# Kernel tuning notes

Measured on AMD Instinct MI355X. Metric: run time of the kernel, lower is better.

Reference implementation:

```python
import jax, jax.numpy as jnp
import numpy as np

S, T, D, H, DQ, F = 2048, 2048, 1024, 16, 1024, 4096
HD = DQ // H


def _layernorm(x, w, b, eps=1e-5):
    mu = jnp.mean(x, axis=-1, keepdims=True)
    var = jnp.mean((x - mu) ** 2, axis=-1, keepdims=True)
    return (x - mu) / jnp.sqrt(var + eps) * w + b


def _attention(q_in, kv_in, mask, wq, bq, wk, bk, wv, bv, wo, bo):
    # q_in: [Sq, D], kv_in: [Sk, D]
    q = (q_in @ wq + bq).reshape(-1, H, HD).transpose(1, 0, 2)   # [H, Sq, hd]
    k = (kv_in @ wk + bk).reshape(-1, H, HD).transpose(1, 0, 2)  # [H, Sk, hd]
    v = (kv_in @ wv + bv).reshape(-1, H, HD).transpose(1, 0, 2)
    scale = jnp.sqrt(jnp.asarray(HD, dtype=q.dtype))
    scores = jnp.einsum('hqd,hkd->hqk', q, k) / scale            # [H, Sq, Sk]
    if mask is not None:
        scores = jnp.where(mask, scores, jnp.finfo(scores.dtype).min)
    attn = jax.nn.softmax(scores, axis=-1)
    ctx = jnp.einsum('hqk,hkd->hqd', attn, v)                    # [H, Sq, hd]
    ctx = ctx.transpose(1, 0, 2).reshape(-1, H * HD)             # [Sq, DQ]
    return ctx @ wo + bo


def setup_inputs() -> dict:
    key = jax.random.key(0)
    ks = jax.random.split(key, 20)

    def lin(kk, fan_in, shape):
        return jax.random.normal(kk, shape, dtype=jnp.float32) / np.sqrt(fan_in)

    inp = {
        'inputs': jax.random.normal(ks[0], (S, D), dtype=jnp.float32),
        'encoder_outputs': jax.random.normal(ks[1], (T, D), dtype=jnp.float32),
        'self_attention_mask': jnp.tril(jnp.ones((S, S), dtype=bool)),
        'cross_attention_mask': jnp.ones((S, T), dtype=bool),
        'ln1_w': jnp.ones((D,), jnp.float32), 'ln1_b': jnp.zeros((D,), jnp.float32),
        'ln2_w': jnp.ones((D,), jnp.float32), 'ln2_b': jnp.zeros((D,), jnp.float32),
        'ln3_w': jnp.ones((D,), jnp.float32), 'ln3_b': jnp.zeros((D,), jnp.float32),
        'sa_wq': lin(ks[2], D, (D, DQ)), 'sa_bq': jnp.zeros((DQ,), jnp.float32),
        'sa_wk': lin(ks[3], D, (D, DQ)), 'sa_bk': jnp.zeros((DQ,), jnp.float32),
        'sa_wv': lin(ks[4], D, (D, DQ)), 'sa_bv': jnp.zeros((DQ,), jnp.float32),
        'sa_wo': lin(ks[5], DQ, (DQ, D)), 'sa_bo': jnp.zeros((D,), jnp.float32),
        'ca_wq': lin(ks[6], D, (D, DQ)), 'ca_bq': jnp.zeros((DQ,), jnp.float32),
        'ca_wk': lin(ks[7], D, (D, DQ)), 'ca_bk': jnp.zeros((DQ,), jnp.float32),
        'ca_wv': lin(ks[8], D, (D, DQ)), 'ca_bv': jnp.zeros((DQ,), jnp.float32),
        'ca_wo': lin(ks[9], DQ, (DQ, D)), 'ca_bo': jnp.zeros((D,), jnp.float32),
        'mlp_wi': lin(ks[10], D, (D, F)), 'mlp_bi': jnp.zeros((F,), jnp.float32),
        'mlp_wo': lin(ks[11], F, (F, D)), 'mlp_bo': jnp.zeros((D,), jnp.float32),
    }
    return inp


def reference(inputs, encoder_outputs, self_attention_mask, cross_attention_mask,
              ln1_w, ln1_b, ln2_w, ln2_b, ln3_w, ln3_b,
              sa_wq, sa_bq, sa_wk, sa_bk, sa_wv, sa_bv, sa_wo, sa_bo,
              ca_wq, ca_bq, ca_wk, ca_bk, ca_wv, ca_bv, ca_wo, ca_bo,
              mlp_wi, mlp_bi, mlp_wo, mlp_bo):
    # pre-norm self-attention
    n1 = _layernorm(inputs, ln1_w, ln1_b)
    x = inputs + _attention(n1, n1, self_attention_mask,
                            sa_wq, sa_bq, sa_wk, sa_bk, sa_wv, sa_bv, sa_wo, sa_bo)
    # pre-norm cross-attention (kv from encoder, not normalized)
    n2 = _layernorm(x, ln2_w, ln2_b)
    x = x + _attention(n2, encoder_outputs, cross_attention_mask,
                       ca_wq, ca_bq, ca_wk, ca_bk, ca_wv, ca_bv, ca_wo, ca_bo)
    # pre-norm MLP
    n3 = _layernorm(x, ln3_w, ln3_b)
    h = jax.nn.relu(n3 @ mlp_wi + mlp_bi)
    return x + (h @ mlp_wo + mlp_bo)
```

## Files before the change

### kernel.cpp

```cpp
#include <hip/hip_runtime.h>


#define S_LEN 2048
#define T_LEN 2048
#define D_DIM 1024
#define H_NUM 16
#define DQ_DIM 1024
#define F_DIM 4096
#define HD_DIM 64

typedef _Float16 f16x8 __attribute__((ext_vector_type(8)));
typedef _Float16 f16x4 __attribute__((ext_vector_type(4)));
typedef float f32x4 __attribute__((ext_vector_type(4)));

__device__ __forceinline__ void split1(float x, _Float16& h, _Float16& l) {
    _Float16 hh = (_Float16)x;
    h = hh;
    l = (_Float16)((x - (float)hh) * 2048.0f);
}

__device__ __forceinline__ void gload16(const void* g, void* l) {
    __builtin_amdgcn_global_load_lds(
        (const __attribute__((address_space(1))) void*)g,
        (__attribute__((address_space(3))) void*)l, 16, 0, 0);
}

struct WC8 { const float* w[8]; _Float16* th[8]; _Float16* tl[8]; };

__global__ __launch_bounds__(256)
void wconv_kernel(WC8 a, int K, int N) {
    __shared__ __align__(16) _Float16 th[64][72], tl[64][72];
    const float* W = a.w[blockIdx.z];
    _Float16* Th = a.th[blockIdx.z];
    _Float16* Tl = a.tl[blockIdx.z];
    int n0 = blockIdx.x * 64, k0 = blockIdx.y * 64;
    int t = threadIdx.x;
#pragma unroll
    for (int i = 0; i < 4; ++i) {
        int idx = i * 256 + t;
        int kk = idx >> 4, nq = idx & 15;
        float4 w4 = *(const float4*)(W + (size_t)(k0 + kk) * N + n0 + nq * 4);
        _Float16 h, l;
        split1(w4.x, h, l); th[nq * 4 + 0][kk] = h; tl[nq * 4 + 0][kk] = l;
        split1(w4.y, h, l); th[nq * 4 + 1][kk] = h; tl[nq * 4 + 1][kk] = l;
        split1(w4.z, h, l); th[nq * 4 + 2][kk] = h; tl[nq * 4 + 2][kk] = l;
        split1(w4.w, h, l); th[nq * 4 + 3][kk] = h; tl[nq * 4 + 3][kk] = l;
    }
    __syncthreads();
#pragma unroll
    for (int i = 0; i < 2; ++i) {
        int idx = i * 256 + t;
        int nn = idx >> 3, kq = idx & 7;
        *(f16x8*)(Th + (size_t)(n0 + nn) * K + k0 + kq * 8) = *(const f16x8*)&th[nn][kq * 8];
        *(f16x8*)(Tl + (size_t)(n0 + nn) * K + k0 + kq * 8) = *(const f16x8*)&tl[nn][kq * 8];
    }
}

__global__ __launch_bounds__(256)
void esplit_kernel(const float* __restrict__ x, _Float16* __restrict__ hi,
                   _Float16* __restrict__ lo) {
    size_t i = ((size_t)blockIdx.x * 256 + threadIdx.x) * 4;
    float4 v = *(const float4*)(x + i);
    f16x4 hv, lv; _Float16 h, l;
    split1(v.x, h, l); hv[0] = h; lv[0] = l;
    split1(v.y, h, l); hv[1] = h; lv[1] = l;
    split1(v.z, h, l); hv[2] = h; lv[2] = l;
    split1(v.w, h, l); hv[3] = h; lv[3] = l;
    *(f16x4*)(hi + i) = hv;
    *(f16x4*)(lo + i) = lv;
}

__global__ __launch_bounds__(256)
void ln_kernel(const float* __restrict__ x, const float* __restrict__ w,
               const float* __restrict__ b, _Float16* __restrict__ outh,
               _Float16* __restrict__ outl) {
    int row = blockIdx.x;
    int t = threadIdx.x;
    float4 v = ((const float4*)(x + (size_t)row * D_DIM))[t];
    float s = v.x + v.y + v.z + v.w;
    float ss = v.x * v.x + v.y * v.y + v.z * v.z + v.w * v.w;
#pragma unroll
    for (int m = 1; m < 64; m <<= 1) {
        s += __shfl_xor(s, m, 64);
        ss += __shfl_xor(ss, m, 64);
    }
    __shared__ float ps[4], pss[4];
    int wid = t >> 6;
    if ((t & 63) == 0) { ps[wid] = s; pss[wid] = ss; }
    __syncthreads();
    s = ps[0] + ps[1] + ps[2] + ps[3];
    ss = pss[0] + pss[1] + pss[2] + pss[3];
    float mu = s * (1.0f / D_DIM);
    float var = ss * (1.0f / D_DIM) - mu * mu;
    float rstd = rsqrtf(var + 1e-5f);
    float4 wv = ((const float4*)w)[t];
    float4 bv = ((const float4*)b)[t];
    f16x4 hv, lv; _Float16 h, l;
    split1((v.x - mu) * rstd * wv.x + bv.x, h, l); hv[0] = h; lv[0] = l;
    split1((v.y - mu) * rstd * wv.y + bv.y, h, l); hv[1] = h; lv[1] = l;
    split1((v.z - mu) * rstd * wv.z + bv.z, h, l); hv[2] = h; lv[2] = l;
    split1((v.w - mu) * rstd * wv.w + bv.w, h, l); hv[3] = h; lv[3] = l;
    *(f16x4*)(outh + (size_t)row * D_DIM + t * 4) = hv;
    *(f16x4*)(outl + (size_t)row * D_DIM + t * 4) = lv;
}

struct GemmArgs {
    const _Float16 *Ah[3], *Al[3];
    const _Float16 *Bh[3], *Bl[3];
    const float *bias[3];
    void *C0[3];
    void *C1[3];
    int trans[3];
};

template <int EPI, int BM>
__global__ __launch_bounds__(256, 2)
void gemm_kernel(GemmArgs ga, int M, int N, int K) {
    static_assert(BM == 64 || BM == 128, "BM");
    constexpr int MI = BM / 32;
    constexpr int ASZ = BM * 32;
    constexpr int BUFSZ = 2 * ASZ + 4096;
    int z = blockIdx.z;
    const _Float16* Ah = ga.Ah[z];
    const _Float16* Al = ga.Al[z];
    const _Float16* Bh = ga.Bh[z];
    const _Float16* Bl = ga.Bl[z];
    const float* bias = ga.bias[z];
    void* C0 = ga.C0[z];
    void* C1 = ga.C1[z];
    int tr = ga.trans[z];

    __shared__ __align__(16) _Float16 lds[2 * BUFSZ];

    int t = threadIdx.x;
    int m0 = blockIdx.y * BM, n0 = blockIdx.x * 64;
    int lane = t & 63, wid = t >> 6;
    int g = lane >> 4, l15 = lane & 15;
    int wm = wid >> 1, wn = wid & 1;

    f32x4 acc1[MI][2] = {};
    f32x4 acc2[MI][2] = {};

    const int nt = K / 32;

    auto stage = [&](int kt, int bi) {
        int k0 = kt * 32;
        _Float16* buf = &lds[bi * BUFSZ];
#pragma unroll
        for (int c = 0; c < BM / 64; ++c) {
            int chunk = c * 256 + t;
            int row = chunk >> 2, cc = chunk & 3;
            int so = k0 + ((cc ^ (row & 3)) << 3);
            gload16(Ah + (size_t)(m0 + row) * K + so, buf + chunk * 8);
            gload16(Al + (size_t)(m0 + row) * K + so, buf + ASZ + chunk * 8);
        }
        {
            int chunk = t;
            int row = chunk >> 2, cc = chunk & 3;
            int so = k0 + ((cc ^ (row & 3)) << 3);
            gload16(Bh + (size_t)(n0 + row) * K + so, buf + 2 * ASZ + chunk * 8);
            gload16(Bl + (size_t)(n0 + row) * K + so, buf + 2 * ASZ + 2048 + chunk * 8);
        }
    };

    stage(0, 0);
    for (int kt = 0; kt < nt; ++kt) {
        __syncthreads();
        if (kt + 1 < nt) stage(kt + 1, (kt + 1) & 1);
        const _Float16* buf = &lds[(kt & 1) * BUFSZ];
        f16x8 ah[MI], al[MI], bh[2], bl[2];
#pragma unroll
        for (int mi = 0; mi < MI; ++mi) {
            int row = wm * (BM / 2) + mi * 16 + l15;
            int cof = row * 32 + ((g ^ (row & 3)) << 3);
            ah[mi] = *(const f16x8*)&buf[cof];
            al[mi] = *(const f16x8*)&buf[ASZ + cof];
        }
#pragma unroll
        for (int ni = 0; ni < 2; ++ni) {
            int row = wn * 32 + ni * 16 + l15;
            int cof = row * 32 + ((g ^ (row & 3)) << 3);
            bh[ni] = *(const f16x8*)&buf[2 * ASZ + cof];
            bl[ni] = *(const f16x8*)&buf[2 * ASZ + 2048 + cof];
        }
#pragma unroll
        for (int mi = 0; mi < MI; ++mi)
#pragma unroll
            for (int ni = 0; ni < 2; ++ni) {
                acc1[mi][ni] = __builtin_amdgcn_mfma_f32_16x16x32_f16(ah[mi], bh[ni], acc1[mi][ni], 0, 0, 0);
                acc2[mi][ni] = __builtin_amdgcn_mfma_f32_16x16x32_f16(ah[mi], bl[ni], acc2[mi][ni], 0, 0, 0);
                acc2[mi][ni] = __builtin_amdgcn_mfma_f32_16x16x32_f16(al[mi], bh[ni], acc2[mi][ni], 0, 0, 0);
            }
    }

#pragma unroll
    for (int ni = 0; ni < 2; ++ni) {
        int col = n0 + wn * 32 + ni * 16 + l15;
        float bb = bias[col];
#pragma unroll
        for (int mi = 0; mi < MI; ++mi) {
            int row0 = m0 + wm * (BM / 2) + mi * 16 + g * 4;
            float vr[4];
#pragma unroll
            for (int r = 0; r < 4; ++r)
                vr[r] = acc1[mi][ni][r] + acc2[mi][ni][r] * (1.0f / 2048.0f) + bb;
            if constexpr (EPI == 0) {
                if (tr) {
                    f16x4 tv;
#pragma unroll
                    for (int r = 0; r < 4; ++r) tv[r] = (_Float16)vr[r];
                    *(f16x4*)((_Float16*)C0 + (size_t)col * M + row0) = tv;
                } else {
#pragma unroll
                    for (int r = 0; r < 4; ++r)
                        ((_Float16*)C0)[(size_t)(row0 + r) * N + col] = (_Float16)vr[r];
                }
            } else if constexpr (EPI == 1) {
#pragma unroll
                for (int r = 0; r < 4; ++r) {
                    size_t off = (size_t)(row0 + r) * N + col;
                    ((float*)C0)[off] = vr[r] + ((const float*)C1)[off];
                }
            } else {
#pragma unroll
                for (int r = 0; r < 4; ++r) {
                    size_t off = (size_t)(row0 + r) * N + col;
                    _Float16 h, l;
                    split1(fmaxf(vr[r], 0.0f), h, l);
                    ((_Float16*)C0)[off] = h;
                    ((_Float16*)C1)[off] = l;
                }
            }
        }
    }
}

template <bool CAUSAL>
__global__ __launch_bounds__(512)
void flash_kernel(const _Float16* __restrict__ Qm, const _Float16* __restrict__ Km,
                  const _Float16* __restrict__ VT, _Float16* __restrict__ Oh,
                  _Float16* __restrict__ Ol, int Sk) {
    __shared__ __align__(16) _Float16 sK[64][64];
    __shared__ __align__(16) _Float16 sVT[64][64];
    __shared__ __align__(16) _Float16 sP[8][16][64];

    int t = threadIdx.x, lane = t & 63, wid = t >> 6;
    int g = lane >> 4, l15 = lane & 15;
    int h = blockIdx.y;
    int NT = Sk / 64;
    int ta = blockIdx.x, tb = NT - 1 - ta;
    int tidx = (wid < 4) ? ta : tb;
    int q0w = tidx * 64 + (wid & 3) * 16;
    int jendw = CAUSAL ? tidx : NT - 1;
    int jend = CAUSAL ? tb : NT - 1;

    f16x8 aq[2];
    {
        const _Float16* qp = Qm + (size_t)(q0w + l15) * DQ_DIM + h * HD_DIM;
#pragma unroll
        for (int ks = 0; ks < 2; ++ks) {
            f16x8 a = *(const f16x8*)(qp + ks * 32 + g * 8);
#pragma unroll
            for (int e = 0; e < 8; ++e) a[e] = a[e] * (_Float16)0.125f;
            aq[ks] = a;
        }
    }

    float m_[4] = {-1e30f, -1e30f, -1e30f, -1e30f};
    float l_[4] = {0.f, 0.f, 0.f, 0.f};
    f32x4 o[4] = {};

    int srow = t >> 3, scc = t & 7;
    f16x8 rk, rv;
    auto loadKV = [&](int jt) {
        int j0 = jt * 64;
        rk = *(const f16x8*)(Km + (size_t)(j0 + srow) * DQ_DIM + h * HD_DIM + scc * 8);
        rv = *(const f16x8*)(VT + (size_t)(h * HD_DIM + srow) * Sk + j0 + scc * 8);
    };

    loadKV(0);
    for (int jt = 0; jt <= jend; ++jt) {
        __syncthreads();
        {
            int sc_ = (scc ^ (srow & 7)) * 8;
            *(f16x8*)&sK[srow][sc_] = rk;
            *(f16x8*)&sVT[srow][sc_] = rv;
        }
        if (jt < jend) loadKV(jt + 1);
        __syncthreads();
        if (jt > jendw) continue;

        int j0 = jt * 64;
        f32x4 sc[4] = {};
#pragma unroll
        for (int cf = 0; cf < 4; ++cf)
#pragma unroll
            for (int ks = 0; ks < 2; ++ks) {
                f16x8 bk = *(const f16x8*)&sK[cf * 16 + l15][((ks * 4 + g) ^ (l15 & 7)) * 8];
                sc[cf] = __builtin_amdgcn_mfma_f32_16x16x32_f16(aq[ks], bk, sc[cf], 0, 0, 0);
            }
        if (CAUSAL && jt == tidx) {
#pragma unroll
            for (int cf = 0; cf < 4; ++cf)
#pragma unroll
                for (int r = 0; r < 4; ++r)
                    if (j0 + cf * 16 + l15 > q0w + g * 4 + r) sc[cf][r] = -1e30f;
        }
#pragma unroll
        for (int r = 0; r < 4; ++r) {
            float tmax = fmaxf(fmaxf(sc[0][r], sc[1][r]), fmaxf(sc[2][r], sc[3][r]));
#pragma unroll
            for (int mm = 1; mm < 16; mm <<= 1) tmax = fmaxf(tmax, __shfl_xor(tmax, mm, 64));
            float mn = fmaxf(m_[r], tmax);
            float corr = __expf(m_[r] - mn);
            float rs = 0.0f;
#pragma unroll
            for (int cf = 0; cf < 4; ++cf) {
                float p = __expf(sc[cf][r] - mn);
                sc[cf][r] = p;
                rs += p;
            }
#pragma unroll
            for (int mm = 1; mm < 16; mm <<= 1) rs += __shfl_xor(rs, mm, 64);
            l_[r] = l_[r] * corr + rs;
            m_[r] = mn;
#pragma unroll
            for (int hf = 0; hf < 4; ++hf) o[hf][r] *= corr;
        }
#pragma unroll
        for (int cf = 0; cf < 4; ++cf)
#pragma unroll
            for (int r = 0; r < 4; ++r) {
                int e = cf * 16 + l15;
                int se = (((e >> 3) ^ ((g * 4 + r) & 7)) << 3) | (e & 7);
                sP[wid][g * 4 + r][se] = (_Float16)sc[cf][r];
            }
#pragma unroll
        for (int ks = 0; ks < 2; ++ks) {
            f16x8 ap = *(const f16x8*)&sP[wid][l15][((ks * 4 + g) ^ (l15 & 7)) * 8];
#pragma unroll
            for (int hf = 0; hf < 4; ++hf) {
                f16x8 bv = *(const f16x8*)&sVT[hf * 16 + l15][((ks * 4 + g) ^ (l15 & 7)) * 8];
                o[hf] = __builtin_amdgcn_mfma_f32_16x16x32_f16(ap, bv, o[hf], 0, 0, 0);
            }
        }
    }

#pragma unroll
    for (int hf = 0; hf < 4; ++hf)
#pragma unroll
        for (int r = 0; r < 4; ++r) {
            int row = q0w + g * 4 + r;
            int col = h * HD_DIM + hf * 16 + l15;
            _Float16 hh, ll;
            split1(o[hf][r] / l_[r], hh, ll);
            Oh[(size_t)row * DQ_DIM + col] = hh;
            Ol[(size_t)row * DQ_DIM + col] = ll;
        }
}

#define MB(x) ((size_t)(x) * 1024 * 1024)

extern "C" void kernel_launch(void* const* d_in, const int* in_sizes, int n_in,
                              void* d_out, int out_size, void* d_ws, size_t ws_size,
                              hipStream_t stream) {
    const float* x_in = (const float*)d_in[0];
    const float* enc  = (const float*)d_in[1];
    const float* ln1w = (const float*)d_in[4];  const float* ln1b = (const float*)d_in[5];
    const float* ln2w = (const float*)d_in[6];  const float* ln2b = (const float*)d_in[7];
    const float* ln3w = (const float*)d_in[8];  const float* ln3b = (const float*)d_in[9];
    const float* sa_wq = (const float*)d_in[10]; const float* sa_bq = (const float*)d_in[11];
    const float* sa_wk = (const float*)d_in[12]; const float* sa_bk = (const float*)d_in[13];
    const float* sa_wv = (const float*)d_in[14]; const float* sa_bv = (const float*)d_in[15];
    const float* sa_wo = (const float*)d_in[16]; const float* sa_bo = (const float*)d_in[17];
    const float* ca_wq = (const float*)d_in[18]; const float* ca_bq = (const float*)d_in[19];
    const float* ca_wk = (const float*)d_in[20]; const float* ca_bk = (const float*)d_in[21];
    const float* ca_wv = (const float*)d_in[22]; const float* ca_bv = (const float*)d_in[23];
    const float* ca_wo = (const float*)d_in[24]; const float* ca_bo = (const float*)d_in[25];
    const float* mlp_wi = (const float*)d_in[26]; const float* mlp_bi = (const float*)d_in[27];
    const float* mlp_wo = (const float*)d_in[28]; const float* mlp_bo = (const float*)d_in[29];
    float* out = (float*)d_out;

    char* base = (char*)d_ws;
    float* X        = (float*)(base + MB(0));
    _Float16* Nbh   = (_Float16*)(base + MB(8));
    _Float16* Nbl   = (_Float16*)(base + MB(12));
    _Float16* Qb    = (_Float16*)(base + MB(16));
    _Float16* Kb    = (_Float16*)(base + MB(20));
    _Float16* VTb   = (_Float16*)(base + MB(24));
    _Float16* CXh   = (_Float16*)(base + MB(28));
    _Float16* CXl   = (_Float16*)(base + MB(32));
    _Float16* wT[8][2];
    const float* wsrc[8] = {sa_wq, sa_wk, sa_wv, sa_wo, ca_wq, ca_wk, ca_wv, ca_wo};
    for (int i = 0; i < 8; ++i) {
        wT[i][0] = (_Float16*)(base + MB(36 + 4 * i));
        wT[i][1] = (_Float16*)(base + MB(36 + 4 * i) + MB(2));
    }
    _Float16* wiTh  = (_Float16*)(base + MB(68));
    _Float16* wiTl  = (_Float16*)(base + MB(76));
    _Float16* woTh  = (_Float16*)(base + MB(84));
    _Float16* woTl  = (_Float16*)(base + MB(92));
    _Float16* ench  = (_Float16*)(base + MB(100));
    _Float16* encl  = (_Float16*)(base + MB(104));
    _Float16* Hbh   = (_Float16*)(base + MB(36));
    _Float16* Hbl   = (_Float16*)(base + MB(52));

    dim3 blk(256);
    dim3 fblk(512);

    {
        WC8 a;
        for (int i = 0; i < 8; ++i) { a.w[i] = wsrc[i]; a.th[i] = wT[i][0]; a.tl[i] = wT[i][1]; }
        wconv_kernel<<<dim3(16, 16, 8), blk, 0, stream>>>(a, D_DIM, DQ_DIM);
    }
    {
        WC8 a = {};
        a.w[0] = mlp_wi; a.th[0] = wiTh; a.tl[0] = wiTl;
        wconv_kernel<<<dim3(F_DIM / 64, D_DIM / 64, 1), blk, 0, stream>>>(a, D_DIM, F_DIM);
    }
    {
        WC8 a = {};
        a.w[0] = mlp_wo; a.th[0] = woTh; a.tl[0] = woTl;
        wconv_kernel<<<dim3(D_DIM / 64, F_DIM / 64, 1), blk, 0, stream>>>(a, F_DIM, D_DIM);
    }
    esplit_kernel<<<(size_t)T_LEN * D_DIM / 1024, blk, 0, stream>>>(enc, ench, encl);

    ln_kernel<<<S_LEN, blk, 0, stream>>>(x_in, ln1w, ln1b, Nbh, Nbl);
    {
        GemmArgs a = {};
        for (int z = 0; z < 3; ++z) { a.Ah[z] = Nbh; a.Al[z] = Nbl; }
        a.Bh[0] = wT[0][0]; a.Bl[0] = wT[0][1]; a.bias[0] = sa_bq; a.C0[0] = Qb;
        a.Bh[1] = wT[1][0]; a.Bl[1] = wT[1][1]; a.bias[1] = sa_bk; a.C0[1] = Kb;
        a.Bh[2] = wT[2][0]; a.Bl[2] = wT[2][1]; a.bias[2] = sa_bv; a.C0[2] = VTb;
        a.trans[2] = 1;
        gemm_kernel<0, 128><<<dim3(DQ_DIM / 64, S_LEN / 128, 3), blk, 0, stream>>>(
            a, S_LEN, DQ_DIM, D_DIM);
    }
    flash_kernel<true><<<dim3(S_LEN / 128, H_NUM), fblk, 0, stream>>>(Qb, Kb, VTb, CXh, CXl, S_LEN);
    {
        GemmArgs a = {};
        a.Ah[0] = CXh; a.Al[0] = CXl;
        a.Bh[0] = wT[3][0]; a.Bl[0] = wT[3][1]; a.bias[0] = sa_bo;
        a.C0[0] = X; a.C1[0] = (void*)x_in;
        gemm_kernel<1, 64><<<dim3(D_DIM / 64, S_LEN / 64, 1), blk, 0, stream>>>(
            a, S_LEN, D_DIM, DQ_DIM);
    }

    ln_kernel<<<S_LEN, blk, 0, stream>>>(X, ln2w, ln2b, Nbh, Nbl);
    {
        GemmArgs a = {};
        a.Ah[0] = Nbh;  a.Al[0] = Nbl;
        a.Ah[1] = ench; a.Al[1] = encl;
        a.Ah[2] = ench; a.Al[2] = encl;
        a.Bh[0] = wT[4][0]; a.Bl[0] = wT[4][1]; a.bias[0] = ca_bq; a.C0[0] = Qb;
        a.Bh[1] = wT[5][0]; a.Bl[1] = wT[5][1]; a.bias[1] = ca_bk; a.C0[1] = Kb;
        a.Bh[2] = wT[6][0]; a.Bl[2] = wT[6][1]; a.bias[2] = ca_bv; a.C0[2] = VTb;
        a.trans[2] = 1;
        gemm_kernel<0, 128><<<dim3(DQ_DIM / 64, S_LEN / 128, 3), blk, 0, stream>>>(
            a, S_LEN, DQ_DIM, D_DIM);
    }
    flash_kernel<false><<<dim3(S_LEN / 128, H_NUM), fblk, 0, stream>>>(Qb, Kb, VTb, CXh, CXl, T_LEN);
    {
        GemmArgs a = {};
        a.Ah[0] = CXh; a.Al[0] = CXl;
        a.Bh[0] = wT[7][0]; a.Bl[0] = wT[7][1]; a.bias[0] = ca_bo;
        a.C0[0] = X; a.C1[0] = X;
        gemm_kernel<1, 64><<<dim3(D_DIM / 64, S_LEN / 64, 1), blk, 0, stream>>>(
            a, S_LEN, D_DIM, DQ_DIM);
    }

    ln_kernel<<<S_LEN, blk, 0, stream>>>(X, ln3w, ln3b, Nbh, Nbl);
    {
        GemmArgs a = {};
        a.Ah[0] = Nbh; a.Al[0] = Nbl;
        a.Bh[0] = wiTh; a.Bl[0] = wiTl; a.bias[0] = mlp_bi;
        a.C0[0] = Hbh; a.C1[0] = Hbl;
        gemm_kernel<2, 128><<<dim3(F_DIM / 64, S_LEN / 128, 1), blk, 0, stream>>>(
            a, S_LEN, F_DIM, D_DIM);
    }
    {
        GemmArgs a = {};
        a.Ah[0] = Hbh; a.Al[0] = Hbl;
        a.Bh[0] = woTh; a.Bl[0] = woTl; a.bias[0] = mlp_bo;
        a.C0[0] = out; a.C1[0] = X;
        gemm_kernel<1, 64><<<dim3(D_DIM / 64, S_LEN / 64, 1), blk, 0, stream>>>(
            a, S_LEN, D_DIM, F_DIM);
    }

    (void)in_sizes; (void)n_in; (void)out_size; (void)ws_size;
}
```

Baseline: 576.4 us.

## Use 128x128 GEMM tiles and split-K for output projections with reduce kernel

Enlarges every GEMM tile to 128x128, with a 4x4 MFMA sub-tile per wave, to raise operand reuse from LDS. The LDS swizzle changes to match. The N=1024 output projections (attention out and MLP down) become a two-way split-K writing fp32 partials. A new elementwise kernel then adds the partials, the bias and the residual. This keeps enough blocks for occupancy with the larger tiles, at the cost of extra partial-sum memory traffic, one more launch and higher register pressure.

Measured after the change: 585.0 us. No clear change (+1.5%).

```diff
diff --git a/kernel.cpp b/kernel.cpp
--- a/kernel.cpp
+++ b/kernel.cpp
@@ -113,53 +113,48 @@
     int trans[3];
 };
 
-template <int EPI, int BM>
+template <int EPI>
 __global__ __launch_bounds__(256, 2)
 void gemm_kernel(GemmArgs ga, int M, int N, int K) {
-    static_assert(BM == 64 || BM == 128, "BM");
-    constexpr int MI = BM / 32;
-    constexpr int ASZ = BM * 32;
-    constexpr int BUFSZ = 2 * ASZ + 4096;
     int z = blockIdx.z;
-    const _Float16* Ah = ga.Ah[z];
-    const _Float16* Al = ga.Al[z];
-    const _Float16* Bh = ga.Bh[z];
-    const _Float16* Bl = ga.Bl[z];
-    const float* bias = ga.bias[z];
-    void* C0 = ga.C0[z];
-    void* C1 = ga.C1[z];
-    int tr = ga.trans[z];
-
-    __shared__ __align__(16) _Float16 lds[2 * BUFSZ];
+    int zi = (EPI == 3) ? 0 : z;
+    const _Float16* Ah = ga.Ah[zi];
+    const _Float16* Al = ga.Al[zi];
+    const _Float16* Bh = ga.Bh[zi];
+    const _Float16* Bl = ga.Bl[zi];
+    const float* bias = ga.bias[zi];
+    void* C0 = ga.C0[zi];
+    void* C1 = ga.C1[zi];
+    int tr = ga.trans[zi];
+
+    int kbeg = 0, klen = K;
+    if constexpr (EPI == 3) { klen = K / 2; kbeg = z * klen; }
+
+    __shared__ __align__(16) _Float16 lds[2][4][4096];
 
     int t = threadIdx.x;
-    int m0 = blockIdx.y * BM, n0 = blockIdx.x * 64;
+    int m0 = blockIdx.y * 128, n0 = blockIdx.x * 128;
     int lane = t & 63, wid = t >> 6;
     int g = lane >> 4, l15 = lane & 15;
     int wm = wid >> 1, wn = wid & 1;
 
-    f32x4 acc1[MI][2] = {};
-    f32x4 acc2[MI][2] = {};
-
-    const int nt = K / 32;
+    f32x4 acc1[4][4] = {};
+    f32x4 acc2[4][4] = {};
+
+    const int nt = klen / 32;
 
     auto stage = [&](int kt, int bi) {
-        int k0 = kt * 32;
-        _Float16* buf = &lds[bi * BUFSZ];
-#pragma unroll
-        for (int c = 0; c < BM / 64; ++c) {
-            int chunk = c * 256 + t;
+        int k0 = kbeg + kt * 32;
+#pragma unroll
+        for (int i = 0; i < 2; ++i) {
+            int chunk = i * 256 + t;
             int row = chunk >> 2, cc = chunk & 3;
-            int so = k0 + ((cc ^ (row & 3)) << 3);
-            gload16(Ah + (size_t)(m0 + row) * K + so, buf + chunk * 8);
-            gload16(Al + (size_t)(m0 + row) * K + so, buf + ASZ + chunk * 8);
-        }
-        {
-            int chunk = t;
-            int row = chunk >> 2, cc = chunk & 3;
-            int so = k0 + ((cc ^ (row & 3)) << 3);
-            gload16(Bh + (size_t)(n0 + row) * K + so, buf + 2 * ASZ + chunk * 8);
-            gload16(Bl + (size_t)(n0 + row) * K + so, buf + 2 * ASZ + 2048 + chunk * 8);
+            int swz = (row ^ (row >> 2)) & 3;
+            int so = k0 + ((cc ^ swz) << 3);
+            gload16(Ah + (size_t)(m0 + row) * K + so, &lds[bi][0][chunk * 8]);
+            gload16(Al + (size_t)(m0 + row) * K + so, &lds[bi][1][chunk * 8]);
+            gload16(Bh + (size_t)(n0 + row) * K + so, &lds[bi][2][chunk * 8]);
+            gload16(Bl + (size_t)(n0 + row) * K + so, &lds[bi][3][chunk * 8]);
         }
     };
 
@@ -167,39 +162,42 @@
     for (int kt = 0; kt < nt; ++kt) {
         __syncthreads();
         if (kt + 1 < nt) stage(kt + 1, (kt + 1) & 1);
-        const _Float16* buf = &lds[(kt & 1) * BUFSZ];
-        f16x8 ah[MI], al[MI], bh[2], bl[2];
-#pragma unroll
-        for (int mi = 0; mi < MI; ++mi) {
-            int row = wm * (BM / 2) + mi * 16 + l15;
-            int cof = row * 32 + ((g ^ (row & 3)) << 3);
-            ah[mi] = *(const f16x8*)&buf[cof];
-            al[mi] = *(const f16x8*)&buf[ASZ + cof];
-        }
-#pragma unroll
-        for (int ni = 0; ni < 2; ++ni) {
-            int row = wn * 32 + ni * 16 + l15;
-            int cof = row * 32 + ((g ^ (row & 3)) << 3);
-            bh[ni] = *(const f16x8*)&buf[2 * ASZ + cof];
-            bl[ni] = *(const f16x8*)&buf[2 * ASZ + 2048 + cof];
-        }
-#pragma unroll
-        for (int mi = 0; mi < MI; ++mi)
-#pragma unroll
-            for (int ni = 0; ni < 2; ++ni) {
+        int bi = kt & 1;
+        f16x8 ah[4], al[4], bh[4], bl[4];
+#pragma unroll
+        for (int mi = 0; mi < 4; ++mi) {
+            int row = wm * 64 + mi * 16 + l15;
+            int cof = row * 32 + ((g ^ ((row ^ (row >> 2)) & 3)) << 3);
+            ah[mi] = *(const f16x8*)&lds[bi][0][cof];
+            al[mi] = *(const f16x8*)&lds[bi][1][cof];
+        }
+#pragma unroll
+        for (int ni = 0; ni < 4; ++ni) {
+            int row = wn * 64 + ni * 16 + l15;
+            int cof = row * 32 + ((g ^ ((row ^ (row >> 2)) & 3)) << 3);
+            bh[ni] = *(const f16x8*)&lds[bi][2][cof];
+            bl[ni] = *(const f16x8*)&lds[bi][3][cof];
+        }
+#pragma unroll
+        for (int mi = 0; mi < 4; ++mi)
+#pragma unroll
+            for (int ni = 0; ni < 4; ++ni) {
                 acc1[mi][ni] = __builtin_amdgcn_mfma_f32_16x16x32_f16(ah[mi], bh[ni], acc1[mi][ni], 0, 0, 0);
                 acc2[mi][ni] = __builtin_amdgcn_mfma_f32_16x16x32_f16(ah[mi], bl[ni], acc2[mi][ni], 0, 0, 0);
                 acc2[mi][ni] = __builtin_amdgcn_mfma_f32_16x16x32_f16(al[mi], bh[ni], acc2[mi][ni], 0, 0, 0);
             }
     }
 
-#pragma unroll
-    for (int ni = 0; ni < 2; ++ni) {
-        int col = n0 + wn * 32 + ni * 16 + l15;
-        float bb = bias[col];
-#pragma unroll
-        for (int mi = 0; mi < MI; ++mi) {
-            int row0 = m0 + wm * (BM / 2) + mi * 16 + g * 4;
+    float* Cp = nullptr;
+    if constexpr (EPI == 3) Cp = (float*)ga.C0[0] + (size_t)z * M * N;
+
+#pragma unroll
+    for (int ni = 0; ni < 4; ++ni) {
+        int col = n0 + wn * 64 + ni * 16 + l15;
+        float bb = (EPI == 3) ? 0.0f : bias[col];
+#pragma unroll
+        for (int mi = 0; mi < 4; ++mi) {
+            int row0 = m0 + wm * 64 + mi * 16 + g * 4;
             float vr[4];
 #pragma unroll
             for (int r = 0; r < 4; ++r)
@@ -215,13 +213,7 @@
                     for (int r = 0; r < 4; ++r)
                         ((_Float16*)C0)[(size_t)(row0 + r) * N + col] = (_Float16)vr[r];
                 }
-            } else if constexpr (EPI == 1) {
-#pragma unroll
-                for (int r = 0; r < 4; ++r) {
-                    size_t off = (size_t)(row0 + r) * N + col;
-                    ((float*)C0)[off] = vr[r] + ((const float*)C1)[off];
-                }
-            } else {
+            } else if constexpr (EPI == 2) {
 #pragma unroll
                 for (int r = 0; r < 4; ++r) {
                     size_t off = (size_t)(row0 + r) * N + col;
@@ -230,9 +222,30 @@
                     ((_Float16*)C0)[off] = h;
                     ((_Float16*)C1)[off] = l;
                 }
+            } else {
+#pragma unroll
+                for (int r = 0; r < 4; ++r)
+                    Cp[(size_t)(row0 + r) * N + col] = vr[r];
             }
         }
     }
+}
+
+__global__ __launch_bounds__(256)
+void rk_kernel(const float* __restrict__ p, const float* __restrict__ bias,
+               const float* __restrict__ res, float* __restrict__ out,
+               int N, size_t MN) {
+    size_t i = ((size_t)blockIdx.x * 256 + threadIdx.x) * 4;
+    float4 a = *(const float4*)(p + i);
+    float4 b = *(const float4*)(p + MN + i);
+    float4 bs = *(const float4*)(bias + (int)(i % N));
+    float4 rv = *(const float4*)(res + i);
+    float4 o;
+    o.x = a.x + b.x + bs.x + rv.x;
+    o.y = a.y + b.y + bs.y + rv.y;
+    o.z = a.z + b.z + bs.z + rv.z;
+    o.w = a.w + b.w + bs.w + rv.w;
+    *(float4*)(out + i) = o;
 }
 
 template <bool CAUSAL>
@@ -390,6 +403,7 @@
     _Float16* VTb   = (_Float16*)(base + MB(24));
     _Float16* CXh   = (_Float16*)(base + MB(28));
     _Float16* CXl   = (_Float16*)(base + MB(32));
+    float* Pk       = (float*)(base + MB(8));
     _Float16* wT[8][2];
     const float* wsrc[8] = {sa_wq, sa_wk, sa_wv, sa_wo, ca_wq, ca_wk, ca_wv, ca_wo};
     for (int i = 0; i < 8; ++i) {
@@ -407,6 +421,7 @@
 
     dim3 blk(256);
     dim3 fblk(512);
+    const size_t SDm = (size_t)S_LEN * D_DIM;
 
     {
         WC8 a;
@@ -433,17 +448,17 @@
         a.Bh[1] = wT[1][0]; a.Bl[1] = wT[1][1]; a.bias[1] = sa_bk; a.C0[1] = Kb;
         a.Bh[2] = wT[2][0]; a.Bl[2] = wT[2][1]; a.bias[2] = sa_bv; a.C0[2] = VTb;
         a.trans[2] = 1;
-        gemm_kernel<0, 128><<<dim3(DQ_DIM / 64, S_LEN / 128, 3), blk, 0, stream>>>(
+        gemm_kernel<0><<<dim3(DQ_DIM / 128, S_LEN / 128, 3), blk, 0, stream>>>(
             a, S_LEN, DQ_DIM, D_DIM);
     }
     flash_kernel<true><<<dim3(S_LEN / 128, H_NUM), fblk, 0, stream>>>(Qb, Kb, VTb, CXh, CXl, S_LEN);
     {
         GemmArgs a = {};
         a.Ah[0] = CXh; a.Al[0] = CXl;
-        a.Bh[0] = wT[3][0]; a.Bl[0] = wT[3][1]; a.bias[0] = sa_bo;
-        a.C0[0] = X; a.C1[0] = (void*)x_in;
-        gemm_kernel<1, 64><<<dim3(D_DIM / 64, S_LEN / 64, 1), blk, 0, stream>>>(
+        a.Bh[0] = wT[3][0]; a.Bl[0] = wT[3][1]; a.C0[0] = Pk;
+        gemm_kernel<3><<<dim3(D_DIM / 128, S_LEN / 128, 2), blk, 0, stream>>>(
             a, S_LEN, D_DIM, DQ_DIM);
+        rk_kernel<<<SDm / 1024, blk, 0, stream>>>(Pk, sa_bo, x_in, X, D_DIM, SDm);
     }
 
     ln_kernel<<<S_LEN, blk, 0, stream>>>(X, ln2w, ln2b, Nbh, Nbl);
@@ -456,17 +471,17 @@
         a.Bh[1] = wT[5][0]; a.Bl[1] = wT[5][1]; a.bias[1] = ca_bk; a.C0[1] = Kb;
         a.Bh[2] = wT[6][0]; a.Bl[2] = wT[6][1]; a.bias[2] = ca_bv; a.C0[2] = VTb;
         a.trans[2] = 1;
-        gemm_kernel<0, 128><<<dim3(DQ_DIM / 64, S_LEN / 128, 3), blk, 0, stream>>>(
+        gemm_kernel<0><<<dim3(DQ_DIM / 128, S_LEN / 128, 3), blk, 0, stream>>>(
             a, S_LEN, DQ_DIM, D_DIM);
     }
     flash_kernel<false><<<dim3(S_LEN / 128, H_NUM), fblk, 0, stream>>>(Qb, Kb, VTb, CXh, CXl, T_LEN);
     {
         GemmArgs a = {};
         a.Ah[0] = CXh; a.Al[0] = CXl;
-        a.Bh[0] = wT[7][0]; a.Bl[0] = wT[7][1]; a.bias[0] = ca_bo;
-        a.C0[0] = X; a.C1[0] = X;
-        gemm_kernel<1, 64><<<dim3(D_DIM / 64, S_LEN / 64, 1), blk, 0, stream>>>(
+        a.Bh[0] = wT[7][0]; a.Bl[0] = wT[7][1]; a.C0[0] = Pk;
+        gemm_kernel<3><<<dim3(D_DIM / 128, S_LEN / 128, 2), blk, 0, stream>>>(
             a, S_LEN, D_DIM, DQ_DIM);
+        rk_kernel<<<SDm / 1024, blk, 0, stream>>>(Pk, ca_bo, X, X, D_DIM, SDm);
     }
 
     ln_kernel<<<S_LEN, blk, 0, stream>>>(X, ln3w, ln3b, Nbh, Nbl);
@@ -475,16 +490,16 @@
         a.Ah[0] = Nbh; a.Al[0] = Nbl;
         a.Bh[0] = wiTh; a.Bl[0] = wiTl; a.bias[0] = mlp_bi;
         a.C0[0] = Hbh; a.C1[0] = Hbl;
-        gemm_kernel<2, 128><<<dim3(F_DIM / 64, S_LEN / 128, 1), blk, 0, stream>>>(
+        gemm_kernel<2><<<dim3(F_DIM / 128, S_LEN / 128, 1), blk, 0, stream>>>(
             a, S_LEN, F_DIM, D_DIM);
     }
     {
         GemmArgs a = {};
         a.Ah[0] = Hbh; a.Al[0] = Hbl;
-        a.Bh[0] = woTh; a.Bl[0] = woTl; a.bias[0] = mlp_bo;
-        a.C0[0] = out; a.C1[0] = X;
-        gemm_kernel<1, 64><<<dim3(D_DIM / 64, S_LEN / 64, 1), blk, 0, stream>>>(
+        a.Bh[0] = woTh; a.Bl[0] = woTl; a.C0[0] = Pk;
+        gemm_kernel<3><<<dim3(D_DIM / 128, S_LEN / 128, 2), blk, 0, stream>>>(
             a, S_LEN, D_DIM, F_DIM);
+        rk_kernel<<<SDm / 1024, blk, 0, stream>>>(Pk, mlp_bo, X, out, D_DIM, SDm);
     }
 
     (void)in_sizes; (void)n_in; (void)out_size; (void)ws_size;
```
